# Kernel tuning notes

Hardware: AMD Instinct MI355X
Metric: run time of the kernel (lower is better)

The kernel has to match this reference:

```python
import jax, jax.numpy as jnp
import numpy as np

TOPK = 9
NUM_CLASSES = 80
IMG = 640
STRIDES = (8, 16, 32)
EPS_IOU = 1e-6   # mmdet BboxOverlaps2D union clamp
EPS_GT = 1e-9    # select_candidates_in_gts eps


def _make_anchors():
    boxes, levels = [], []
    for s in STRIDES:
        n = IMG // s
        c = (np.arange(n, dtype=np.float32) + 0.5) * s
        cx, cy = np.meshgrid(c, c)
        ctr = np.stack([cx.ravel(), cy.ravel()], -1)
        half = 2.5 * s
        boxes.append(np.concatenate([ctr - half, ctr + half], -1))
        levels.append(n * n)
    return np.concatenate(boxes, 0).astype(np.float32), np.array(levels, np.int64)


def setup_inputs() -> dict:
    key = jax.random.key(0)
    ks = jax.random.split(key, 6)
    bs, n_max = 32, 64
    anc, levels = _make_anchors()
    A = anc.shape[0]
    xy = jax.random.uniform(ks[0], (bs, n_max, 2)) * 560.0
    wh = jax.random.uniform(ks[1], (bs, n_max, 2)) * 120.0 + 8.0
    gt_bboxes = jnp.concatenate([xy, xy + wh], -1)
    pxy = jax.random.uniform(ks[2], (bs, A, 2)) * 560.0
    pwh = jax.random.uniform(ks[3], (bs, A, 2)) * 120.0 + 8.0
    pd_bboxes = jnp.concatenate([pxy, pxy + pwh], -1)
    gt_labels = jax.random.randint(ks[4], (bs, n_max, 1), 0, NUM_CLASSES)
    mask_gt = (jax.random.uniform(ks[5], (bs, n_max, 1)) < 0.8).astype(jnp.float32)
    return {"anc_bboxes": jnp.asarray(anc), "n_level_bboxes": levels,
            "gt_labels": gt_labels, "gt_bboxes": gt_bboxes,
            "mask_gt": mask_gt, "pd_bboxes": pd_bboxes}


def _assign(anc_bboxes, levels, gt_labels, gt_bboxes, mask_gt, pd_bboxes):
    A = anc_bboxes.shape[0]
    bs, n_max, _ = gt_bboxes.shape
    gt_flat = gt_bboxes.reshape(-1, 4)
    # pairwise IoU gt vs anchors (mmdet BboxOverlaps2D), (bs, n_max, A)
    lt = jnp.maximum(gt_flat[:, None, :2], anc_bboxes[None, :, :2])
    rb = jnp.minimum(gt_flat[:, None, 2:], anc_bboxes[None, :, 2:])
    inter = jnp.clip(rb - lt, 0).prod(-1)
    area_g = jnp.clip(gt_flat[:, 2:] - gt_flat[:, :2], 0).prod(-1)
    area_a = jnp.clip(anc_bboxes[:, 2:] - anc_bboxes[:, :2], 0).prod(-1)
    union = jnp.maximum(area_g[:, None] + area_a[None, :] - inter, EPS_IOU)
    overlaps = (inter / union).reshape(bs, n_max, A)
    # center distances, (bs, n_max, A)
    gt_c = (gt_flat[:, :2] + gt_flat[:, 2:]) * 0.5
    ac_c = (anc_bboxes[:, :2] + anc_bboxes[:, 2:]) * 0.5
    dist = jnp.sqrt(((gt_c[:, None, :] - ac_c[None, :, :]) ** 2).sum(-1)).reshape(bs, n_max, A)
    # per-level topk (smallest distance) candidates
    mask_gt_b = mask_gt > 0  # (bs, n_max, 1)
    row = jnp.arange(bs * n_max)[:, None]
    is_in_list, idx_list = [], []
    start = 0
    for L in levels:
        k = min(TOPK, L)
        d = dist[..., start:start + L]
        _, idxs = jax.lax.top_k(-d, k)  # (bs, n_max, k)
        idx_list.append(idxs + start)
        idxs_m = jnp.where(mask_gt_b, idxs, 0).reshape(bs * n_max, k)
        cnt = jnp.zeros((bs * n_max, L), dist.dtype).at[row, idxs_m].add(1.0)
        cnt = cnt.reshape(bs, n_max, L)
        is_in_list.append(jnp.where(cnt > 1, jnp.zeros_like(cnt), cnt))
        start += L
    is_in_candidate = jnp.concatenate(is_in_list, -1)  # (bs, n_max, A)
    candidate_idxs = jnp.concatenate(idx_list, -1)     # (bs, n_max, n_levels*k)
    # ATSS threshold = mean + std (unbiased) over candidate overlaps
    cand_ov_full = jnp.where(is_in_candidate > 0, overlaps, jnp.zeros_like(overlaps))
    cand = jnp.take_along_axis(cand_ov_full.reshape(bs * n_max, A),
                               candidate_idxs.reshape(bs * n_max, -1), axis=1)
    cand = cand.reshape(bs, n_max, -1)
    thr = cand.mean(-1, keepdims=True) + cand.std(-1, keepdims=True, ddof=1)
    is_pos = jnp.where(cand_ov_full > thr, is_in_candidate, jnp.zeros_like(is_in_candidate))
    # anchor centers strictly inside gt boxes
    deltas = jnp.concatenate([ac_c[None, None] - gt_bboxes[:, :, None, :2],
                              gt_bboxes[:, :, None, 2:] - ac_c[None, None]], -1)
    is_in_gts = (deltas.min(-1) > EPS_GT).astype(dist.dtype)
    mask_pos = is_pos * is_in_gts * mask_gt  # (bs, n_max, A)
    # resolve anchors assigned to multiple gts by highest IoU (always applied; no-op if no conflicts)
    fg_mask = mask_pos.sum(1)  # (bs, A)
    multi = fg_mask[:, None, :] > 1
    is_max = jnp.transpose(jax.nn.one_hot(overlaps.argmax(1), n_max, dtype=overlaps.dtype), (0, 2, 1))
    mask_pos = jnp.where(multi, is_max, mask_pos)
    fg_mask = mask_pos.sum(1)
    target_gt_idx = mask_pos.argmax(1)  # (bs, A)
    # gather targets
    flat_idx = (target_gt_idx + jnp.arange(bs)[:, None] * n_max).reshape(-1)
    target_labels = gt_labels.reshape(-1)[flat_idx].reshape(bs, A)
    target_labels = jnp.where(fg_mask > 0, target_labels, NUM_CLASSES)
    target_bboxes = gt_flat[flat_idx].reshape(bs, A, 4)
    target_scores = jax.nn.one_hot(target_labels, NUM_CLASSES + 1, dtype=overlaps.dtype)[..., :NUM_CLASSES]
    # scale scores by IoU(gt, pred) of the assigned gt
    lt2 = jnp.maximum(gt_bboxes[:, :, None, :2], pd_bboxes[:, None, :, :2])
    rb2 = jnp.minimum(gt_bboxes[:, :, None, 2:], pd_bboxes[:, None, :, 2:])
    ov2 = jnp.clip(rb2 - lt2, 0).prod(-1)
    a1 = jnp.clip(gt_bboxes[:, :, 2:] - gt_bboxes[:, :, :2], 0).prod(-1)[:, :, None]
    a2 = jnp.clip(pd_bboxes[:, :, 2:] - pd_bboxes[:, :, :2], 0).prod(-1)[:, None, :]
    ious = ov2 / (a1 + a2 - ov2 + 1e-9) * mask_pos
    target_scores = target_scores * jnp.max(ious, axis=1)[..., None]
    return target_labels.astype(jnp.int32), target_bboxes, target_scores, fg_mask > 0


def reference(anc_bboxes, n_level_bboxes, gt_labels, gt_bboxes, mask_gt, pd_bboxes):
    levels = [int(v) for v in np.asarray(n_level_bboxes)]
    return _assign(anc_bboxes, levels, gt_labels, gt_bboxes, mask_gt, pd_bboxes)
```

## Files before the change

kernel.cpp:

```cpp
#include <hip/hip_runtime.h>
#include <stdint.h>

#pragma clang fp contract(off)

#define BS 32
#define NMAX 64
#define A_TOT 8400
#define NC 80


template<int N, int S, int START, int C0>
__device__ __forceinline__ void do_level(
    float gcx, float gcy,
    float x1, float y1, float x2, float y2, float area_g,
    int (&aidx)[27], float (&ov)[27], float (&acxA)[27], float (&acyA)[27])
{
  unsigned long long kk[9];
#pragma unroll
  for (int i = 0; i < 9; ++i) kk[i] = ~0ULL;
  const float s = (float)S;
  int j0 = (int)floorf(gcx / s);
  int i0 = (int)floorf(gcy / s);
  int jlo = min(max(j0 - 2, 0), N - 5);
  int ilo = min(max(i0 - 2, 0), N - 5);
#pragma unroll
  for (int di = 0; di < 5; ++di) {
    int ii = ilo + di;
    float ay = ((float)ii + 0.5f) * s;
    float dy = gcy - ay;
    float dy2 = dy * dy;
#pragma unroll
    for (int dj = 0; dj < 5; ++dj) {
      int jj = jlo + dj;
      float ax = ((float)jj + 0.5f) * s;
      float dx = gcx - ax;
      float d = sqrtf(dx * dx + dy2);
      unsigned long long key =
          ((unsigned long long)__float_as_uint(d) << 32) |
          (unsigned int)(START + ii * N + jj);
      if (key < kk[8]) {
        kk[8] = key;
#pragma unroll
        for (int t = 8; t > 0; --t) {
          unsigned long long lo = kk[t], hi = kk[t - 1];
          if (lo < hi) { kk[t] = hi; kk[t - 1] = lo; }
        }
      }
    }
  }
#pragma unroll
  for (int t = 0; t < 9; ++t) {
    int a = (int)(kk[t] & 0xffffffffULL);
    int loc = a - START;
    int ii = loc / N;
    int jj = loc - ii * N;
    float cx = ((float)jj + 0.5f) * s;
    float cy = ((float)ii + 0.5f) * s;
    const float h = 2.5f * (float)S;
    float ax1 = cx - h, ay1 = cy - h, ax2 = cx + h, ay2 = cy + h;
    float iw = fminf(x2, ax2) - fmaxf(x1, ax1); iw = fmaxf(iw, 0.f);
    float ih = fminf(y2, ay2) - fmaxf(y1, ay1); ih = fmaxf(ih, 0.f);
    float inter = iw * ih;
    float area_a = fmaxf(ax2 - ax1, 0.f) * fmaxf(ay2 - ay1, 0.f);
    float uni = fmaxf(area_g + area_a - inter, 1e-6f);
    ov[C0 + t] = inter / uni;
    aidx[C0 + t] = a;
    acxA[C0 + t] = cx;
    acyA[C0 + t] = cy;
  }
}

__global__ __launch_bounds__(256) void atss_assign_k(
    const float* __restrict__ gt_bboxes,
    const float* __restrict__ mask_gt,
    int* __restrict__ cnt, int* __restrict__ ming)
{
  int t = blockIdx.x * 256 + threadIdx.x;
  if (t >= BS * NMAX) return;
  if (!(mask_gt[t] > 0.0f)) return;
  int b = t >> 6;
  int g = t & 63;
  const float* gb = gt_bboxes + (size_t)t * 4;
  float x1 = gb[0], y1 = gb[1], x2 = gb[2], y2 = gb[3];
  float gcx = (x1 + x2) * 0.5f;
  float gcy = (y1 + y2) * 0.5f;
  float area_g = fmaxf(x2 - x1, 0.f) * fmaxf(y2 - y1, 0.f);

  int aidx[27];
  float ov[27], acxA[27], acyA[27];
  do_level<80,  8,    0,  0>(gcx, gcy, x1, y1, x2, y2, area_g, aidx, ov, acxA, acyA);
  do_level<40, 16, 6400,  9>(gcx, gcy, x1, y1, x2, y2, area_g, aidx, ov, acxA, acyA);
  do_level<20, 32, 8000, 18>(gcx, gcy, x1, y1, x2, y2, area_g, aidx, ov, acxA, acyA);

  float sum = 0.f;
#pragma unroll
  for (int c = 0; c < 27; ++c) sum += ov[c];
  float mean = sum / 27.f;
  float ss = 0.f;
#pragma unroll
  for (int c = 0; c < 27; ++c) { float d = ov[c] - mean; ss += d * d; }
  float thr = mean + sqrtf(ss / 26.f);

#pragma unroll
  for (int c = 0; c < 27; ++c) {
    if (ov[c] > thr) {
      float m = fminf(fminf(acxA[c] - x1, acyA[c] - y1),
                      fminf(x2 - acxA[c], y2 - acyA[c]));
      if (m > 1e-9f) {
        int idx = b * A_TOT + aidx[c];
        atomicAdd(&cnt[idx], 1);
        atomicMin(&ming[idx], g);
      }
    }
  }
}


__global__ __launch_bounds__(256) void atss_finalize_k(
    const float* __restrict__ anc,
    const int* __restrict__ gt_labels,
    const float* __restrict__ gt_bboxes,
    const float* __restrict__ pd_bboxes,
    const int* __restrict__ cnt,
    const int* __restrict__ ming,
    float* __restrict__ out)
{
  __shared__ float s_gt[NMAX * 4];
  __shared__ int   s_lab[NMAX];
  __shared__ int   s_alab[256];
  __shared__ float s_as[256];

  const int b   = blockIdx.y;
  const int a0  = blockIdx.x * 256;
  const int tid = threadIdx.x;

  s_gt[tid] = gt_bboxes[(size_t)b * NMAX * 4 + tid];
  if (tid < NMAX) s_lab[tid] = gt_labels[b * NMAX + tid];
  __syncthreads();

  const int a = a0 + tid;
  int lab = NC; float sc = 0.f; int gsel = 0; int fg = 0;

  if (a < A_TOT) {
    const int ia = b * A_TOT + a;
    const int c = cnt[ia];
    if (c == 1) { gsel = ming[ia]; fg = 1; }
    else if (c > 1) {
      const float* ab = anc + (size_t)a * 4;
      float ax1 = ab[0], ay1 = ab[1], ax2 = ab[2], ay2 = ab[3];
      float area_a = fmaxf(ax2 - ax1, 0.f) * fmaxf(ay2 - ay1, 0.f);
      float best = -1.f; int bg = 0;
      for (int gg = 0; gg < NMAX; ++gg) {
        float x1 = s_gt[gg * 4 + 0], y1 = s_gt[gg * 4 + 1];
        float x2 = s_gt[gg * 4 + 2], y2 = s_gt[gg * 4 + 3];
        float iw = fminf(x2, ax2) - fmaxf(x1, ax1); iw = fmaxf(iw, 0.f);
        float ih = fminf(y2, ay2) - fmaxf(y1, ay1); ih = fmaxf(ih, 0.f);
        float inter = iw * ih;
        float ag = fmaxf(x2 - x1, 0.f) * fmaxf(y2 - y1, 0.f);
        float uni = fmaxf(ag + area_a - inter, 1e-6f);
        float iou = inter / uni;
        if (iou > best) { best = iou; bg = gg; }
      }
      gsel = bg; fg = 1;
    }

    if (fg) {
      lab = s_lab[gsel];
      float x1 = s_gt[gsel * 4 + 0], y1 = s_gt[gsel * 4 + 1];
      float x2 = s_gt[gsel * 4 + 2], y2 = s_gt[gsel * 4 + 3];
      const float4 pb = *(const float4*)(pd_bboxes + (size_t)ia * 4);
      float iw = fminf(x2, pb.z) - fmaxf(x1, pb.x); iw = fmaxf(iw, 0.f);
      float ih = fminf(y2, pb.w) - fmaxf(y1, pb.y); ih = fmaxf(ih, 0.f);
      float inter = iw * ih;
      float ag = fmaxf(x2 - x1, 0.f) * fmaxf(y2 - y1, 0.f);
      float ap = fmaxf(pb.z - pb.x, 0.f) * fmaxf(pb.w - pb.y, 0.f);
      sc = inter / (ag + ap - inter + 1e-9f);
    }

    out[ia] = (float)lab;
    float4 bb = { s_gt[gsel*4+0], s_gt[gsel*4+1], s_gt[gsel*4+2], s_gt[gsel*4+3] };
    *(float4*)(out + (size_t)BS * A_TOT + (size_t)ia * 4) = bb;
    out[(size_t)BS * A_TOT * 85 + ia] = fg ? 1.0f : 0.0f;
  }

  s_alab[tid] = lab;
  s_as[tid]   = sc;
  __syncthreads();

  const int na = min(256, A_TOT - a0);
  float* outS = out + (size_t)BS * A_TOT * 5 + ((size_t)b * A_TOT + a0) * NC;
  const int nv4 = na * (NC / 4);
  for (int i = tid; i < nv4; i += 256) {
    int al = i / (NC / 4);
    int c4 = (i - al * (NC / 4)) * 4;
    int L  = s_alab[al];
    float s = s_as[al];
    float4 v;
    v.x = (L == c4 + 0) ? s : 0.f;
    v.y = (L == c4 + 1) ? s : 0.f;
    v.z = (L == c4 + 2) ? s : 0.f;
    v.w = (L == c4 + 3) ? s : 0.f;
    ((float4*)outS)[i] = v;
  }
}


extern "C" void kernel_launch(void* const* d_in, const int* in_sizes, int n_in,
                              void* d_out, int out_size, void* d_ws, size_t ws_size,
                              hipStream_t stream) {
  const float* anc       = (const float*)d_in[0];
  const int*   gt_labels = (const int*)  d_in[2];
  const float* gt_bboxes = (const float*)d_in[3];
  const float* mask_gt   = (const float*)d_in[4];
  const float* pd_bboxes = (const float*)d_in[5];
  float* out = (float*)d_out;

  int* cnt  = (int*)d_ws;
  int* ming = cnt + BS * A_TOT;

  hipMemsetAsync(cnt,  0,    BS * A_TOT * sizeof(int), stream);
  hipMemsetAsync(ming, 0x7f, BS * A_TOT * sizeof(int), stream);

  atss_assign_k<<<dim3((BS * NMAX + 255) / 256), 256, 0, stream>>>(
      gt_bboxes, mask_gt, cnt, ming);

  atss_finalize_k<<<dim3((A_TOT + 255) / 256, BS), 256, 0, stream>>>(
      anc, gt_labels, gt_bboxes, pd_bboxes, cnt, ming, out);
}
```

Measured before the change: 134.7 us.

## Fuse assignment and finalize into one kernel with per-block shared-memory candidate scatter

Drops the two workspace memsets and the separate per-GT assign kernel. Each finalize block now recomputes candidate selection for the GTs whose 5x5 windows overlap its anchor range, and scatters counts and minimum-GT indices into shared memory instead of global atomics. Anchor coordinates are computed analytically instead of read from memory, and the pred-box load is hoisted. In exchange, top-k selection is recomputed redundantly across blocks, only 64 threads of each block do that serial work, and shared-memory use grows.

```diff
diff --git a/kernel.cpp b/kernel.cpp
--- a/kernel.cpp
+++ b/kernel.cpp
@@ -8,21 +8,16 @@
 #define A_TOT 8400
 #define NC 80
 
-
 template<int N, int S, int START, int C0>
-__device__ __forceinline__ void do_level(
-    float gcx, float gcy,
+__device__ __forceinline__ void select_and_iou(
+    int ilo, int jlo, float gcx, float gcy,
     float x1, float y1, float x2, float y2, float area_g,
-    int (&aidx)[27], float (&ov)[27], float (&acxA)[27], float (&acyA)[27])
+    float* __restrict__ ovrow, int* __restrict__ idxrow)
 {
   unsigned long long kk[9];
 #pragma unroll
   for (int i = 0; i < 9; ++i) kk[i] = ~0ULL;
   const float s = (float)S;
-  int j0 = (int)floorf(gcx / s);
-  int i0 = (int)floorf(gcy / s);
-  int jlo = min(max(j0 - 2, 0), N - 5);
-  int ilo = min(max(i0 - 2, 0), N - 5);
 #pragma unroll
   for (int di = 0; di < 5; ++di) {
     int ii = ilo + di;
@@ -50,8 +45,8 @@
   }
 #pragma unroll
   for (int t = 0; t < 9; ++t) {
-    int a = (int)(kk[t] & 0xffffffffULL);
-    int loc = a - START;
+    int aa = (int)(kk[t] & 0xffffffffULL);
+    int loc = aa - START;
     int ii = loc / N;
     int jj = loc - ii * N;
     float cx = ((float)jj + 0.5f) * s;
@@ -63,91 +58,128 @@
     float inter = iw * ih;
     float area_a = fmaxf(ax2 - ax1, 0.f) * fmaxf(ay2 - ay1, 0.f);
     float uni = fmaxf(area_g + area_a - inter, 1e-6f);
-    ov[C0 + t] = inter / uni;
-    aidx[C0 + t] = a;
-    acxA[C0 + t] = cx;
-    acyA[C0 + t] = cy;
-  }
-}
-
-__global__ __launch_bounds__(256) void atss_assign_k(
+    ovrow[C0 + t] = inter / uni;
+    idxrow[C0 + t] = aa;
+  }
+}
+
+template<int N, int S, int START, int C0>
+__device__ __forceinline__ void scatter_level(
+    const float* __restrict__ ovrow, const int* __restrict__ idxrow,
+    float thr, float x1, float y1, float x2, float y2,
+    int a0, int na, int g, int* s_cnt, int* s_gmin)
+{
+  const float s = (float)S;
+#pragma unroll
+  for (int t = 0; t < 9; ++t) {
+    float o = ovrow[C0 + t];
+    if (o > thr) {
+      int aa = idxrow[C0 + t];
+      if (aa >= a0 && aa < a0 + na) {
+        int loc = aa - START;
+        int ii = loc / N;
+        int jj = loc - ii * N;
+        float cx = ((float)jj + 0.5f) * s;
+        float cy = ((float)ii + 0.5f) * s;
+        float m = fminf(fminf(cx - x1, cy - y1), fminf(x2 - cx, y2 - cy));
+        if (m > 1e-9f) {
+          atomicAdd(&s_cnt[aa - a0], 1);
+          atomicMin(&s_gmin[aa - a0], g);
+        }
+      }
+    }
+  }
+}
+
+
+__global__ __launch_bounds__(256) void atss_fused_k(
+    const int* __restrict__ gt_labels,
     const float* __restrict__ gt_bboxes,
     const float* __restrict__ mask_gt,
-    int* __restrict__ cnt, int* __restrict__ ming)
-{
-  int t = blockIdx.x * 256 + threadIdx.x;
-  if (t >= BS * NMAX) return;
-  if (!(mask_gt[t] > 0.0f)) return;
-  int b = t >> 6;
-  int g = t & 63;
-  const float* gb = gt_bboxes + (size_t)t * 4;
-  float x1 = gb[0], y1 = gb[1], x2 = gb[2], y2 = gb[3];
-  float gcx = (x1 + x2) * 0.5f;
-  float gcy = (y1 + y2) * 0.5f;
-  float area_g = fmaxf(x2 - x1, 0.f) * fmaxf(y2 - y1, 0.f);
-
-  int aidx[27];
-  float ov[27], acxA[27], acyA[27];
-  do_level<80,  8,    0,  0>(gcx, gcy, x1, y1, x2, y2, area_g, aidx, ov, acxA, acyA);
-  do_level<40, 16, 6400,  9>(gcx, gcy, x1, y1, x2, y2, area_g, aidx, ov, acxA, acyA);
-  do_level<20, 32, 8000, 18>(gcx, gcy, x1, y1, x2, y2, area_g, aidx, ov, acxA, acyA);
-
-  float sum = 0.f;
-#pragma unroll
-  for (int c = 0; c < 27; ++c) sum += ov[c];
-  float mean = sum / 27.f;
-  float ss = 0.f;
-#pragma unroll
-  for (int c = 0; c < 27; ++c) { float d = ov[c] - mean; ss += d * d; }
-  float thr = mean + sqrtf(ss / 26.f);
-
-#pragma unroll
-  for (int c = 0; c < 27; ++c) {
-    if (ov[c] > thr) {
-      float m = fminf(fminf(acxA[c] - x1, acyA[c] - y1),
-                      fminf(x2 - acxA[c], y2 - acyA[c]));
-      if (m > 1e-9f) {
-        int idx = b * A_TOT + aidx[c];
-        atomicAdd(&cnt[idx], 1);
-        atomicMin(&ming[idx], g);
-      }
-    }
-  }
-}
-
-
-__global__ __launch_bounds__(256) void atss_finalize_k(
-    const float* __restrict__ anc,
-    const int* __restrict__ gt_labels,
-    const float* __restrict__ gt_bboxes,
     const float* __restrict__ pd_bboxes,
-    const int* __restrict__ cnt,
-    const int* __restrict__ ming,
     float* __restrict__ out)
 {
   __shared__ float s_gt[NMAX * 4];
   __shared__ int   s_lab[NMAX];
+  __shared__ float s_ov[NMAX][27];
+  __shared__ int   s_idx[NMAX][27];
+  __shared__ int   s_cnt[256];
+  __shared__ int   s_gmin[256];
   __shared__ int   s_alab[256];
-  __shared__ float s_as[256];
+  __shared__ float s_asc[256];
 
   const int b   = blockIdx.y;
   const int a0  = blockIdx.x * 256;
+  const int na  = min(256, A_TOT - a0);
   const int tid = threadIdx.x;
 
   s_gt[tid] = gt_bboxes[(size_t)b * NMAX * 4 + tid];
   if (tid < NMAX) s_lab[tid] = gt_labels[b * NMAX + tid];
+  s_cnt[tid]  = 0;
+  s_gmin[tid] = NMAX;
+  __syncthreads();
+
+  if (tid < NMAX) {
+    const int g = tid;
+    if (mask_gt[b * NMAX + g] > 0.0f) {
+      float x1 = s_gt[g * 4 + 0], y1 = s_gt[g * 4 + 1];
+      float x2 = s_gt[g * 4 + 2], y2 = s_gt[g * 4 + 3];
+      float gcx = (x1 + x2) * 0.5f;
+      float gcy = (y1 + y2) * 0.5f;
+
+      int jlo0 = min(max((int)floorf(gcx / 8.f)  - 2, 0), 80 - 5);
+      int ilo0 = min(max((int)floorf(gcy / 8.f)  - 2, 0), 80 - 5);
+      int jlo1 = min(max((int)floorf(gcx / 16.f) - 2, 0), 40 - 5);
+      int ilo1 = min(max((int)floorf(gcy / 16.f) - 2, 0), 40 - 5);
+      int jlo2 = min(max((int)floorf(gcx / 32.f) - 2, 0), 20 - 5);
+      int ilo2 = min(max((int)floorf(gcy / 32.f) - 2, 0), 20 - 5);
+
+      int lo0 = ilo0 * 80 + jlo0,          hi0 = (ilo0 + 4) * 80 + jlo0 + 4;
+      int lo1 = 6400 + ilo1 * 40 + jlo1,   hi1 = 6400 + (ilo1 + 4) * 40 + jlo1 + 4;
+      int lo2 = 8000 + ilo2 * 20 + jlo2,   hi2 = 8000 + (ilo2 + 4) * 20 + jlo2 + 4;
+      bool act = (lo0 < a0 + na && hi0 >= a0) ||
+                 (lo1 < a0 + na && hi1 >= a0) ||
+                 (lo2 < a0 + na && hi2 >= a0);
+
+      if (act) {
+        float area_g = fmaxf(x2 - x1, 0.f) * fmaxf(y2 - y1, 0.f);
+        float* ovrow = s_ov[g];
+        int*   idxrow = s_idx[g];
+        select_and_iou<80,  8,    0,  0>(ilo0, jlo0, gcx, gcy, x1, y1, x2, y2, area_g, ovrow, idxrow);
+        select_and_iou<40, 16, 6400,  9>(ilo1, jlo1, gcx, gcy, x1, y1, x2, y2, area_g, ovrow, idxrow);
+        select_and_iou<20, 32, 8000, 18>(ilo2, jlo2, gcx, gcy, x1, y1, x2, y2, area_g, ovrow, idxrow);
+
+        float sum = 0.f;
+#pragma unroll
+        for (int c = 0; c < 27; ++c) sum += ovrow[c];
+        float mean = sum / 27.f;
+        float ss = 0.f;
+#pragma unroll
+        for (int c = 0; c < 27; ++c) { float d = ovrow[c] - mean; ss += d * d; }
+        float thr = mean + sqrtf(ss / 26.f);
+
+        scatter_level<80,  8,    0,  0>(ovrow, idxrow, thr, x1, y1, x2, y2, a0, na, g, s_cnt, s_gmin);
+        scatter_level<40, 16, 6400,  9>(ovrow, idxrow, thr, x1, y1, x2, y2, a0, na, g, s_cnt, s_gmin);
+        scatter_level<20, 32, 8000, 18>(ovrow, idxrow, thr, x1, y1, x2, y2, a0, na, g, s_cnt, s_gmin);
+      }
+    }
+  }
   __syncthreads();
 
   const int a = a0 + tid;
   int lab = NC; float sc = 0.f; int gsel = 0; int fg = 0;
 
   if (a < A_TOT) {
-    const int ia = b * A_TOT + a;
-    const int c = cnt[ia];
-    if (c == 1) { gsel = ming[ia]; fg = 1; }
+    const size_t ia = (size_t)b * A_TOT + a;
+    const float4 pb = *(const float4*)(pd_bboxes + ia * 4);
+    const int c = s_cnt[tid];
+    if (c == 1) { gsel = s_gmin[tid]; fg = 1; }
     else if (c > 1) {
-      const float* ab = anc + (size_t)a * 4;
-      float ax1 = ab[0], ay1 = ab[1], ax2 = ab[2], ay2 = ab[3];
+      float cx, cy, h;
+      if (a < 6400)      { int ii = a / 80;          int jj = a - ii * 80;  cx = ((float)jj + 0.5f) * 8.f;  cy = ((float)ii + 0.5f) * 8.f;  h = 20.f; }
+      else if (a < 8000) { int loc = a - 6400; int ii = loc / 40; int jj = loc - ii * 40; cx = ((float)jj + 0.5f) * 16.f; cy = ((float)ii + 0.5f) * 16.f; h = 40.f; }
+      else               { int loc = a - 8000; int ii = loc / 20; int jj = loc - ii * 20; cx = ((float)jj + 0.5f) * 32.f; cy = ((float)ii + 0.5f) * 32.f; h = 80.f; }
+      float ax1 = cx - h, ay1 = cy - h, ax2 = cx + h, ay2 = cy + h;
       float area_a = fmaxf(ax2 - ax1, 0.f) * fmaxf(ay2 - ay1, 0.f);
       float best = -1.f; int bg = 0;
       for (int gg = 0; gg < NMAX; ++gg) {
@@ -168,7 +200,6 @@
       lab = s_lab[gsel];
       float x1 = s_gt[gsel * 4 + 0], y1 = s_gt[gsel * 4 + 1];
       float x2 = s_gt[gsel * 4 + 2], y2 = s_gt[gsel * 4 + 3];
-      const float4 pb = *(const float4*)(pd_bboxes + (size_t)ia * 4);
       float iw = fminf(x2, pb.z) - fmaxf(x1, pb.x); iw = fmaxf(iw, 0.f);
       float ih = fminf(y2, pb.w) - fmaxf(y1, pb.y); ih = fmaxf(ih, 0.f);
       float inter = iw * ih;
@@ -178,28 +209,28 @@
     }
 
     out[ia] = (float)lab;
-    float4 bb = { s_gt[gsel*4+0], s_gt[gsel*4+1], s_gt[gsel*4+2], s_gt[gsel*4+3] };
-    *(float4*)(out + (size_t)BS * A_TOT + (size_t)ia * 4) = bb;
+    float4 bb = { s_gt[gsel * 4 + 0], s_gt[gsel * 4 + 1],
+                  s_gt[gsel * 4 + 2], s_gt[gsel * 4 + 3] };
+    *(float4*)(out + (size_t)BS * A_TOT + ia * 4) = bb;
     out[(size_t)BS * A_TOT * 85 + ia] = fg ? 1.0f : 0.0f;
   }
 
   s_alab[tid] = lab;
-  s_as[tid]   = sc;
+  s_asc[tid]  = sc;
   __syncthreads();
 
-  const int na = min(256, A_TOT - a0);
   float* outS = out + (size_t)BS * A_TOT * 5 + ((size_t)b * A_TOT + a0) * NC;
   const int nv4 = na * (NC / 4);
   for (int i = tid; i < nv4; i += 256) {
     int al = i / (NC / 4);
     int c4 = (i - al * (NC / 4)) * 4;
     int L  = s_alab[al];
-    float s = s_as[al];
+    float sv = s_asc[al];
     float4 v;
-    v.x = (L == c4 + 0) ? s : 0.f;
-    v.y = (L == c4 + 1) ? s : 0.f;
-    v.z = (L == c4 + 2) ? s : 0.f;
-    v.w = (L == c4 + 3) ? s : 0.f;
+    v.x = (L == c4 + 0) ? sv : 0.f;
+    v.y = (L == c4 + 1) ? sv : 0.f;
+    v.z = (L == c4 + 2) ? sv : 0.f;
+    v.w = (L == c4 + 3) ? sv : 0.f;
     ((float4*)outS)[i] = v;
   }
 }
@@ -208,22 +239,12 @@
 extern "C" void kernel_launch(void* const* d_in, const int* in_sizes, int n_in,
                               void* d_out, int out_size, void* d_ws, size_t ws_size,
                               hipStream_t stream) {
-  const float* anc       = (const float*)d_in[0];
   const int*   gt_labels = (const int*)  d_in[2];
   const float* gt_bboxes = (const float*)d_in[3];
   const float* mask_gt   = (const float*)d_in[4];
   const float* pd_bboxes = (const float*)d_in[5];
   float* out = (float*)d_out;
 
-  int* cnt  = (int*)d_ws;
-  int* ming = cnt + BS * A_TOT;
-
-  hipMemsetAsync(cnt,  0,    BS * A_TOT * sizeof(int), stream);
-  hipMemsetAsync(ming, 0x7f, BS * A_TOT * sizeof(int), stream);
-
-  atss_assign_k<<<dim3((BS * NMAX + 255) / 256), 256, 0, stream>>>(
-      gt_bboxes, mask_gt, cnt, ming);
-
-  atss_finalize_k<<<dim3((A_TOT + 255) / 256, BS), 256, 0, stream>>>(
-      anc, gt_labels, gt_bboxes, pd_bboxes, cnt, ming, out);
-}
+  atss_fused_k<<<dim3((A_TOT + 255) / 256, BS), 256, 0, stream>>>(
+      gt_labels, gt_bboxes, mask_gt, pd_bboxes, out);
+}
```

New measurement: 136.9 us. No clear change (+1.7%).
